# Optimization experiments

Hardware: AMD Instinct MI355X
Metric: run time of the kernel (lower is better)

## Reference

```python
import jax, jax.numpy as jnp
import numpy as np

B, N, T, C = 16, 12, 128, 128  # batch, num_classes (nodes), temporal, channels


def _bn(x, gamma, beta, eps=1e-5):
    # BatchNorm2d in training mode: stats over (batch, t, c), channel axis 1, biased var
    mean = jnp.mean(x, axis=(0, 2, 3), keepdims=True)
    var = jnp.var(x, axis=(0, 2, 3), keepdims=True)
    xn = (x - mean) * jax.lax.rsqrt(var + eps)
    return xn * gamma[None, :, None, None] + beta[None, :, None, None]


def setup_inputs() -> dict:
    key = jax.random.key(0)
    ks = jax.random.split(key, 3)
    scale = np.float32(np.sqrt(2.0 / C))
    inp = {
        'x': jax.random.normal(ks[0], (B, N, T, C), dtype=jnp.float32),
        'edge': jax.random.normal(ks[1], (B, N * N, T, C), dtype=jnp.float32),
    }
    wk = jax.random.split(ks[2], 10)
    for name, k in zip(['A1', 'B1', 'E1', 'U1', 'V1', 'A2', 'B2', 'E2', 'U2', 'V2'], wk):
        inp[name] = jax.random.normal(k, (C, C), dtype=jnp.float32) * scale
    for name, dim in [('g_e1', N * N), ('b_e1', N * N), ('g_v1', N), ('b_v1', N),
                      ('g_e2', N * N), ('b_e2', N * N), ('g_v2', N), ('b_v2', N)]:
        inp[name] = jnp.ones((dim,), jnp.float32) if name[0] == 'g' else jnp.zeros((dim,), jnp.float32)
    return inp


def _forward(x, edge, A1, B1, E1, U1, V1, A2, B2, E2, U2, V2,
             g_e1, b_e1, g_v1, b_v1, g_e2, b_e2, g_v2, b_v2):
    # create_e_matrix: edge index e = i*N + j; 'end' selects node i, 'start' selects node j.
    # Dense incidence einsums become pure gathers; the transpose einsum is a
    # scatter-add over j, i.e. a reshape + sum.
    i_idx = jnp.repeat(jnp.arange(N), N)  # end-node of each edge
    j_idx = jnp.tile(jnp.arange(N), N)    # start-node of each edge
    b, _, t, c = x.shape

    def layer(x, edge, A, Bw, E, U, V, ge, be, gv, bv, mask_node):
        res = x
        edge_upd = (x @ A.T)[:, i_idx] + (x @ Bw.T)[:, j_idx] + edge @ E.T
        edge_upd = _bn(edge_upd, ge, be)
        edge_upd = jnp.where(jnp.isnan(edge_upd), 0.0, edge_upd)
        edge = edge + jax.nn.relu(edge_upd)
        e = jax.nn.sigmoid(edge)
        e = jax.nn.softmax(e.reshape(b, N, N, t, c), axis=2).reshape(b, N * N, t, c)
        Ujx = (x @ V.T)[:, j_idx]
        agg = (e * Ujx).reshape(b, N, N, t, c).sum(axis=2) / N  # scatter to end nodes
        xn = _bn(x @ U.T + agg, gv, bv)
        if mask_node:  # original only NaN-masks node BN in layer 1
            xn = jnp.where(jnp.isnan(xn), 0.0, xn)
        return jax.nn.relu(res + xn), edge

    x, edge = layer(x, edge, A1, B1, E1, U1, V1, g_e1, b_e1, g_v1, b_v1, True)
    x, edge = layer(x, edge, A2, B2, E2, U2, V2, g_e2, b_e2, g_v2, b_v2, False)
    return x, edge


def reference(x, edge, A1, B1, E1, U1, V1, A2, B2, E2, U2, V2,
              g_e1, b_e1, g_v1, b_v1, g_e2, b_e2, g_v2, b_v2):
    return _forward(x, edge, A1, B1, E1, U1, V1, A2, B2, E2, U2, V2,
                    g_e1, b_e1, g_v1, b_v1, g_e2, b_e2, g_v2, b_v2)
```

## Files before the change

kernel.cpp:

```cpp
#include <hip/hip_runtime.h>
#include <hip/hip_bf16.h>

#define BB 16
#define NN 12
#define NE 144
#define TT 128
#define CC 128

typedef __attribute__((ext_vector_type(8))) short v8s;
typedef __attribute__((ext_vector_type(4))) short v4s;
typedef __attribute__((ext_vector_type(4))) float v4f;

__device__ __forceinline__ short f2bf(float f) {
    unsigned u = __float_as_uint(f);
    u += 0x7fffu + ((u >> 16) & 1u);
    return (short)(u >> 16);
}
__device__ __forceinline__ float bf2f(unsigned short u) {
    return __uint_as_float(((unsigned)u) << 16);
}
__device__ __forceinline__ v4s f4_to_bf4(float4 a) {
    v4s r; r[0] = f2bf(a.x); r[1] = f2bf(a.y); r[2] = f2bf(a.z); r[3] = f2bf(a.w); return r;
}

__global__ __launch_bounds__(256) void kW(
    const float* A1, const float* B1, const float* E1, const float* U1, const float* V1,
    const float* A2, const float* B2, const float* E2, const float* U2, const float* V2,
    unsigned short* wb)
{
    int idx = blockIdx.x * 256 + threadIdx.x;
    int w = idx >> 14, r = idx & 16383;
    const float* s;
    switch (w) {
        case 0: s = A1; break; case 1: s = B1; break; case 2: s = E1; break;
        case 3: s = U1; break; case 4: s = V1; break; case 5: s = A2; break;
        case 6: s = B2; break; case 7: s = E2; break; case 8: s = U2; break;
        default: s = V2; break;
    }
    wb[idx] = (unsigned short)f2bf(s[r]);
}

__global__ __launch_bounds__(256) void kP(
    const float* __restrict__ x, const unsigned short* __restrict__ wb,
    int sA, int sB, int sV, int sU,
    unsigned short* __restrict__ oA, unsigned short* __restrict__ oB,
    unsigned short* __restrict__ oV, unsigned short* __restrict__ oU)
{
    __shared__ unsigned short xt[64][136];
    int tid = threadIdx.x;
    int m0 = blockIdx.x * 64;
    #pragma unroll
    for (int it = 0; it < 8; ++it) {
        int f = it * 256 + tid;
        int row = f >> 5, c4 = f & 31;
        float4 v = *reinterpret_cast<const float4*>(x + (size_t)m0 * 128 + (size_t)f * 4);
        *reinterpret_cast<v4s*>(&xt[row][c4 * 4]) = f4_to_bf4(v);
    }
    __syncthreads();
    int lane = tid & 63, wid = tid >> 6;
    int l15 = lane & 15, l4 = lane >> 4;

    const unsigned short* Ws[4] = { wb + (size_t)sA * 16384, wb + (size_t)sB * 16384,
                                    wb + (size_t)sV * 16384, wb + (size_t)sU * 16384 };
    unsigned short* Os[4] = { oA, oB, oV, oU };

    #pragma unroll
    for (int w = 0; w < 4; ++w) {
        const unsigned short* W = Ws[w];
        unsigned short* out = Os[w];
        v8s bfr[2][4];
        #pragma unroll
        for (int nt2 = 0; nt2 < 2; ++nt2) {
            int col = (wid * 2 + nt2) * 16 + l15;
            #pragma unroll
            for (int kk = 0; kk < 4; ++kk)
                bfr[nt2][kk] = *reinterpret_cast<const v8s*>(W + col * 128 + kk * 32 + l4 * 8);
        }
        v4f acc[4][2] = {};
        #pragma unroll
        for (int kk = 0; kk < 4; ++kk) {
            #pragma unroll
            for (int mt = 0; mt < 4; ++mt) {
                v8s a = *reinterpret_cast<const v8s*>(&xt[mt * 16 + l15][kk * 32 + l4 * 8]);
                acc[mt][0] = __builtin_amdgcn_mfma_f32_16x16x32_bf16(a, bfr[0][kk], acc[mt][0], 0, 0, 0);
                acc[mt][1] = __builtin_amdgcn_mfma_f32_16x16x32_bf16(a, bfr[1][kk], acc[mt][1], 0, 0, 0);
            }
        }
        #pragma unroll
        for (int mt = 0; mt < 4; ++mt) {
            #pragma unroll
            for (int nt2 = 0; nt2 < 2; ++nt2) {
                int col = (wid * 2 + nt2) * 16 + l15;
                #pragma unroll
                for (int reg = 0; reg < 4; ++reg) {
                    int rowg = m0 + mt * 16 + l4 * 4 + reg;
                    out[(size_t)rowg * 128 + col] = (unsigned short)f2bf(acc[mt][nt2][reg]);
                }
            }
        }
    }
}

template<bool IN_F32>
__global__ __launch_bounds__(256) void kA(
    const float* __restrict__ ef32, const unsigned short* __restrict__ ebf_in,
    unsigned short* __restrict__ ebf_out,
    unsigned short* __restrict__ updg,
    const unsigned short* __restrict__ xAp, const unsigned short* __restrict__ xBp,
    const unsigned short* __restrict__ Ebf, float2* __restrict__ epart)
{
    __shared__ unsigned short et[64][136];
    __shared__ unsigned short xs[64][136];
    __shared__ float sblk[2];
    int tid = threadIdx.x;
    int bid = blockIdx.x;
    int th = bid & 1;  int m = bid >> 1;
    int e = m % NE, b = m / NE;
    int iA = e / 12, jA = e - iA * 12;
    int t0 = th * 64;
    if (tid < 2) sblk[tid] = 0.f;

    size_t erow0 = ((size_t)(b * NE + e) * TT + t0) * CC;
    if constexpr (IN_F32) {
        #pragma unroll
        for (int it = 0; it < 8; ++it) {
            int f = it * 256 + tid;
            int row = f >> 5, c4 = f & 31;
            float4 v = *reinterpret_cast<const float4*>(ef32 + erow0 + (size_t)row * CC + c4 * 4);
            *reinterpret_cast<v4s*>(&et[row][c4 * 4]) = f4_to_bf4(v);
        }
    } else {
        #pragma unroll
        for (int it = 0; it < 4; ++it) {
            int f = it * 256 + tid;
            int row = f >> 4, c8 = f & 15;
            *reinterpret_cast<v8s*>(&et[row][c8 * 8]) =
                *reinterpret_cast<const v8s*>(ebf_in + erow0 + (size_t)row * CC + c8 * 8);
        }
    }
    {
        size_t xarow = ((size_t)(b * NN + iA) * TT + t0) * CC;
        size_t xbrow = ((size_t)(b * NN + jA) * TT + t0) * CC;
        #pragma unroll
        for (int it = 0; it < 4; ++it) {
            int f = it * 256 + tid;
            int row = f >> 4, c8 = f & 15;
            v8s av = *reinterpret_cast<const v8s*>(xAp + xarow + (size_t)row * CC + c8 * 8);
            v8s bv = *reinterpret_cast<const v8s*>(xBp + xbrow + (size_t)row * CC + c8 * 8);
            v8s sv;
            #pragma unroll
            for (int k = 0; k < 8; ++k)
                sv[k] = f2bf(bf2f((unsigned short)av[k]) + bf2f((unsigned short)bv[k]));
            *reinterpret_cast<v8s*>(&xs[row][c8 * 8]) = sv;
        }
    }
    __syncthreads();
    if constexpr (IN_F32) {
        #pragma unroll
        for (int it = 0; it < 4; ++it) {
            int f = it * 256 + tid;
            int row = f >> 4, c8 = f & 15;
            *reinterpret_cast<v8s*>(ebf_out + erow0 + (size_t)row * CC + c8 * 8) =
                *reinterpret_cast<const v8s*>(&et[row][c8 * 8]);
        }
    }
    int lane = tid & 63, wid = tid >> 6;
    int l15 = lane & 15, l4 = lane >> 4;
    v8s bfr[2][4];
    #pragma unroll
    for (int nt2 = 0; nt2 < 2; ++nt2) {
        int col = (wid * 2 + nt2) * 16 + l15;
        #pragma unroll
        for (int kk = 0; kk < 4; ++kk)
            bfr[nt2][kk] = *reinterpret_cast<const v8s*>(Ebf + col * 128 + kk * 32 + l4 * 8);
    }
    v4f acc[4][2] = {};
    #pragma unroll
    for (int kk = 0; kk < 4; ++kk) {
        #pragma unroll
        for (int mt = 0; mt < 4; ++mt) {
            v8s a = *reinterpret_cast<const v8s*>(&et[mt * 16 + l15][kk * 32 + l4 * 8]);
            acc[mt][0] = __builtin_amdgcn_mfma_f32_16x16x32_bf16(a, bfr[0][kk], acc[mt][0], 0, 0, 0);
            acc[mt][1] = __builtin_amdgcn_mfma_f32_16x16x32_bf16(a, bfr[1][kk], acc[mt][1], 0, 0, 0);
        }
    }
    float s = 0.f, q = 0.f;
    #pragma unroll
    for (int mt = 0; mt < 4; ++mt) {
        #pragma unroll
        for (int nt2 = 0; nt2 < 2; ++nt2) {
            int col = (wid * 2 + nt2) * 16 + l15;
            #pragma unroll
            for (int reg = 0; reg < 4; ++reg) {
                int row = mt * 16 + l4 * 4 + reg;
                float v = acc[mt][nt2][reg] + bf2f(xs[row][col]);
                s += v; q += v * v;
                updg[erow0 + (size_t)row * CC + col] = (unsigned short)f2bf(v);
            }
        }
    }
    #pragma unroll
    for (int off = 1; off < 64; off <<= 1) { s += __shfl_xor(s, off); q += __shfl_xor(q, off); }
    if (lane == 0) { atomicAdd(&sblk[0], s); atomicAdd(&sblk[1], q); }
    __syncthreads();
    if (tid == 0) epart[bid] = make_float2(sblk[0], sblk[1]);
}

__global__ __launch_bounds__(64) void kRede(
    const float2* __restrict__ epart, const float* __restrict__ g,
    const float* __restrict__ be, float* __restrict__ estats)
{
    int e = blockIdx.x;
    int tid = threadIdx.x;
    float s = 0.f, q = 0.f;
    if (tid < 32) {
        int b = tid >> 1, th = tid & 1;
        float2 p = epart[(size_t)((b * NE + e) * 2 + th)];
        s = p.x; q = p.y;
    }
    #pragma unroll
    for (int off = 1; off < 32; off <<= 1) { s += __shfl_xor(s, off); q += __shfl_xor(q, off); }
    if (tid == 0) {
        const float M = 262144.f;
        float mean = s / M;
        float var = q / M - mean * mean;
        float sc = g[e] * rsqrtf(var + 1e-5f);
        estats[e * 2] = sc;
        estats[e * 2 + 1] = be[e] - mean * sc;
    }
}

template<bool OUT_F32>
__global__ __launch_bounds__(256) void kC(
    unsigned short* __restrict__ ebf,
    float* __restrict__ eout,
    const unsigned short* __restrict__ updg,
    const unsigned short* __restrict__ xV, const unsigned short* __restrict__ xU,
    const float* __restrict__ estats,
    unsigned short* __restrict__ yout, float* __restrict__ npart)
{
    __shared__ unsigned short rb[48][136];
    __shared__ unsigned short xv[12][136];
    __shared__ float2 scf[48];
    __shared__ float ns[4], nq[4];
    int tid = threadIdx.x;
    int bid = blockIdx.x;
    int third = bid % 3; int bt = bid / 3;
    int b = bt >> 7, t = bt & 127;
    if (tid < 48) scf[tid] = make_float2(estats[(third * 48 + tid) * 2],
                                         estats[(third * 48 + tid) * 2 + 1]);
    if (tid < 4) { ns[tid] = 0.f; nq[tid] = 0.f; }
    if (tid < 192) {
        int row = tid >> 4, c8 = tid & 15;
        *reinterpret_cast<v8s*>(&xv[row][c8 * 8]) =
            *reinterpret_cast<const v8s*>(xV + (((size_t)(b * NN + row) * TT) + t) * CC + c8 * 8);
    }
    __syncthreads();
    int lane = tid & 63;
    #pragma unroll
    for (int it = 0; it < 3; ++it) {
        int f = it * 256 + tid;
        int row = f >> 4, c8 = f & 15;
        int eg = third * 48 + row;
        size_t goff = (((size_t)(b * NE + eg) * TT) + t) * CC + c8 * 8;
        v8s uv = *reinterpret_cast<const v8s*>(updg + goff);
        v8s ev = *reinterpret_cast<const v8s*>(ebf + goff);
        float2 sc = scf[row];
        float en[8]; v8s nv;
        #pragma unroll
        for (int k = 0; k < 8; ++k) {
            float bn = fmaxf(sc.x * bf2f((unsigned short)uv[k]) + sc.y, 0.f);
            en[k] = bf2f((unsigned short)ev[k]) + bn;
            nv[k] = f2bf(en[k]);
        }
        *reinterpret_cast<v8s*>(&rb[row][c8 * 8]) = nv;
        if constexpr (OUT_F32) {
            *reinterpret_cast<float4*>(eout + goff)     = make_float4(en[0], en[1], en[2], en[3]);
            *reinterpret_cast<float4*>(eout + goff + 4) = make_float4(en[4], en[5], en[6], en[7]);
        } else {
            *reinterpret_cast<v8s*>(ebf + goff) = nv;
        }
    }
    __syncthreads();
    #pragma unroll
    for (int ph = 0; ph < 2; ++ph) {
        int u = tid + ph * 256;
        int il = u >> 7, c = u & 127;
        float den = 0.f, ag = 0.f;
        #pragma unroll
        for (int j = 0; j < 12; ++j) {
            float sv = bf2f(rb[il * 12 + j][c]);
            float sg = 1.f / (1.f + __expf(-sv));
            float ev = __expf(sg);
            den += ev;
            ag += ev * bf2f(xv[j][c]);
        }
        float agg = ag / (den * 12.f);
        int i = third * 4 + il;
        size_t xa = (((size_t)(b * NN + i) * TT) + t) * CC + c;
        float yv = bf2f(xU[xa]) + agg;
        unsigned short us = (unsigned short)f2bf(yv);
        yout[xa] = us;
        float yr = bf2f(us);
        float s1 = yr, s2 = yr * yr;
        #pragma unroll
        for (int off = 1; off < 64; off <<= 1) { s1 += __shfl_xor(s1, off); s2 += __shfl_xor(s2, off); }
        if (lane == 0) { atomicAdd(&ns[il], s1); atomicAdd(&nq[il], s2); }
    }
    __syncthreads();
    if (tid < 4) {
        npart[(size_t)bid * 8 + tid * 2 + 0] = ns[tid];
        npart[(size_t)bid * 8 + tid * 2 + 1] = nq[tid];
    }
}

__global__ __launch_bounds__(256) void kRedn(
    const float* __restrict__ npart, const float* __restrict__ g,
    const float* __restrict__ be, float* __restrict__ nstats)
{
    int n = blockIdx.x;
    int third = n >> 2, il = n & 3;
    float s = 0.f, q = 0.f;
    for (int bt = threadIdx.x; bt < 2048; bt += 256) {
        const float* p = npart + ((size_t)(bt * 3 + third) * 8 + il * 2);
        s += p[0]; q += p[1];
    }
    __shared__ float ss[4], qq[4];
    #pragma unroll
    for (int off = 32; off >= 1; off >>= 1) { s += __shfl_down(s, off); q += __shfl_down(q, off); }
    int wid = threadIdx.x >> 6;
    if ((threadIdx.x & 63) == 0) { ss[wid] = s; qq[wid] = q; }
    __syncthreads();
    if (threadIdx.x == 0) {
        s = ss[0] + ss[1] + ss[2] + ss[3];
        q = qq[0] + qq[1] + qq[2] + qq[3];
        const float M = 262144.f;
        float mean = s / M;
        float var = q / M - mean * mean;
        float sc = g[n] * rsqrtf(var + 1e-5f);
        nstats[n * 2] = sc;
        nstats[n * 2 + 1] = be[n] - mean * sc;
    }
}

__global__ __launch_bounds__(256) void kE(
    const float* xres, const unsigned short* __restrict__ yin,
    const float* __restrict__ nstats, float* xout)
{
    int idx4 = blockIdx.x * 256 + threadIdx.x;
    size_t base = (size_t)idx4 * 4;
    int n = (int)((base >> 14) % 12);
    float scv = nstats[n * 2], shv = nstats[n * 2 + 1];
    float4 xvv = *reinterpret_cast<const float4*>(xres + base);
    v4s yv4 = *reinterpret_cast<const v4s*>(yin + base);
    float4 o;
    o.x = fmaxf(xvv.x + scv * bf2f((unsigned short)yv4[0]) + shv, 0.f);
    o.y = fmaxf(xvv.y + scv * bf2f((unsigned short)yv4[1]) + shv, 0.f);
    o.z = fmaxf(xvv.z + scv * bf2f((unsigned short)yv4[2]) + shv, 0.f);
    o.w = fmaxf(xvv.w + scv * bf2f((unsigned short)yv4[3]) + shv, 0.f);
    *reinterpret_cast<float4*>(xout + base) = o;
}

extern "C" void kernel_launch(void* const* d_in, const int* in_sizes, int n_in,
                              void* d_out, int out_size, void* d_ws, size_t ws_size,
                              hipStream_t stream)
{
    const float* x0 = (const float*)d_in[0];
    const float* e0 = (const float*)d_in[1];
    const float* W[10];
    for (int i = 0; i < 10; ++i) W[i] = (const float*)d_in[2 + i];
    const float* ge1 = (const float*)d_in[12];
    const float* be1 = (const float*)d_in[13];
    const float* gv1 = (const float*)d_in[14];
    const float* bv1 = (const float*)d_in[15];
    const float* ge2 = (const float*)d_in[16];
    const float* be2 = (const float*)d_in[17];
    const float* gv2 = (const float*)d_in[18];
    const float* bv2 = (const float*)d_in[19];

    const size_t SZX = (size_t)BB * NN * TT * CC;
    const size_t SZE = (size_t)BB * NE * TT * CC;
    float* out_x = (float*)d_out;
    float* out_e = out_x + SZX;

    unsigned short* ws16 = (unsigned short*)d_ws;
    unsigned short* xA = ws16;
    unsigned short* xB = ws16 + SZX;
    unsigned short* xV = ws16 + 2 * SZX;
    unsigned short* xU = ws16 + 3 * SZX;
    unsigned short* yb = ws16 + 4 * SZX;
    unsigned short* ebf = ws16 + 5 * SZX;
    unsigned short* upd = ebf + SZE;
    float2* epart  = (float2*)(upd + SZE);
    float* estats = (float*)(epart + 4608);
    float* npart  = estats + 288;
    float* nstats = npart + 49152;
    unsigned short* wb = (unsigned short*)(nstats + 24);

    float* x1 = out_x;

    kW<<<640, 256, 0, stream>>>(W[0], W[1], W[2], W[3], W[4], W[5], W[6], W[7], W[8], W[9], wb);

    kP<<<384, 256, 0, stream>>>(x0, wb, 0, 1, 4, 3, xA, xB, xV, xU);
    kA<true><<<4608, 256, 0, stream>>>(e0, nullptr, ebf, upd, xA, xB, wb + 2 * 16384, epart);
    kRede<<<144, 64, 0, stream>>>(epart, ge1, be1, estats);
    kC<false><<<6144, 256, 0, stream>>>(ebf, nullptr, upd, xV, xU, estats, yb, npart);
    kRedn<<<12, 256, 0, stream>>>(npart, gv1, bv1, nstats);
    kE<<<3072, 256, 0, stream>>>(x0, yb, nstats, x1);

    kP<<<384, 256, 0, stream>>>(x1, wb, 5, 6, 9, 8, xA, xB, xV, xU);
    kA<false><<<4608, 256, 0, stream>>>(nullptr, ebf, nullptr, upd, xA, xB, wb + 7 * 16384, epart);
    kRede<<<144, 64, 0, stream>>>(epart, ge2, be2, estats);
    kC<true><<<6144, 256, 0, stream>>>(ebf, out_e, upd, xV, xU, estats, yb, npart);
    kRedn<<<12, 256, 0, stream>>>(npart, gv2, bv2, nstats);
    kE<<<3072, 256, 0, stream>>>(x1, yb, nstats, out_x);
}
```

Measured before the change: 297.3 us.

## Transpose edge GEMM in kA, halve tile rows, drop xs staging buffer

The edge-update kernel now processes 32 time rows per block instead of 64, which doubles the grid to 9216 blocks. It swaps the MFMA operand roles so the edge tile in LDS is the B operand and the weight matrix E is read directly from global as the A operand. Each lane then holds 4 contiguous output channels, so updg writes and the xA/xB loads become 8-byte vector accesses. The shared xs buffer and its precomputed sum are removed, and xA+xB are read straight from global in the epilogue, which cuts LDS use and raises occupancy. The trade-offs are repeated global reads of E per block, more partial stats, and a slightly different rounding (xA+xB is no longer rounded to bf16 before the add).

```diff
diff --git a/kernel.cpp b/kernel.cpp
--- a/kernel.cpp
+++ b/kernel.cpp
@@ -109,21 +109,20 @@
     const unsigned short* __restrict__ xAp, const unsigned short* __restrict__ xBp,
     const unsigned short* __restrict__ Ebf, float2* __restrict__ epart)
 {
-    __shared__ unsigned short et[64][136];
-    __shared__ unsigned short xs[64][136];
+    __shared__ unsigned short et[32][136];
     __shared__ float sblk[2];
     int tid = threadIdx.x;
     int bid = blockIdx.x;
-    int th = bid & 1;  int m = bid >> 1;
+    int th = bid & 3; int m = bid >> 2;
     int e = m % NE, b = m / NE;
     int iA = e / 12, jA = e - iA * 12;
-    int t0 = th * 64;
+    int t0 = th * 32;
     if (tid < 2) sblk[tid] = 0.f;
-
     size_t erow0 = ((size_t)(b * NE + e) * TT + t0) * CC;
+
     if constexpr (IN_F32) {
         #pragma unroll
-        for (int it = 0; it < 8; ++it) {
+        for (int it = 0; it < 4; ++it) {
             int f = it * 256 + tid;
             int row = f >> 5, c4 = f & 31;
             float4 v = *reinterpret_cast<const float4*>(ef32 + erow0 + (size_t)row * CC + c4 * 4);
@@ -131,33 +130,17 @@
         }
     } else {
         #pragma unroll
-        for (int it = 0; it < 4; ++it) {
+        for (int it = 0; it < 2; ++it) {
             int f = it * 256 + tid;
             int row = f >> 4, c8 = f & 15;
             *reinterpret_cast<v8s*>(&et[row][c8 * 8]) =
                 *reinterpret_cast<const v8s*>(ebf_in + erow0 + (size_t)row * CC + c8 * 8);
         }
     }
-    {
-        size_t xarow = ((size_t)(b * NN + iA) * TT + t0) * CC;
-        size_t xbrow = ((size_t)(b * NN + jA) * TT + t0) * CC;
-        #pragma unroll
-        for (int it = 0; it < 4; ++it) {
-            int f = it * 256 + tid;
-            int row = f >> 4, c8 = f & 15;
-            v8s av = *reinterpret_cast<const v8s*>(xAp + xarow + (size_t)row * CC + c8 * 8);
-            v8s bv = *reinterpret_cast<const v8s*>(xBp + xbrow + (size_t)row * CC + c8 * 8);
-            v8s sv;
-            #pragma unroll
-            for (int k = 0; k < 8; ++k)
-                sv[k] = f2bf(bf2f((unsigned short)av[k]) + bf2f((unsigned short)bv[k]));
-            *reinterpret_cast<v8s*>(&xs[row][c8 * 8]) = sv;
-        }
-    }
     __syncthreads();
     if constexpr (IN_F32) {
         #pragma unroll
-        for (int it = 0; it < 4; ++it) {
+        for (int it = 0; it < 2; ++it) {
             int f = it * 256 + tid;
             int row = f >> 4, c8 = f & 15;
             *reinterpret_cast<v8s*>(ebf_out + erow0 + (size_t)row * CC + c8 * 8) =
@@ -166,38 +149,41 @@
     }
     int lane = tid & 63, wid = tid >> 6;
     int l15 = lane & 15, l4 = lane >> 4;
-    v8s bfr[2][4];
-    #pragma unroll
-    for (int nt2 = 0; nt2 < 2; ++nt2) {
-        int col = (wid * 2 + nt2) * 16 + l15;
-        #pragma unroll
-        for (int kk = 0; kk < 4; ++kk)
-            bfr[nt2][kk] = *reinterpret_cast<const v8s*>(Ebf + col * 128 + kk * 32 + l4 * 8);
-    }
-    v4f acc[4][2] = {};
-    #pragma unroll
-    for (int kk = 0; kk < 4; ++kk) {
-        #pragma unroll
-        for (int mt = 0; mt < 4; ++mt) {
-            v8s a = *reinterpret_cast<const v8s*>(&et[mt * 16 + l15][kk * 32 + l4 * 8]);
-            acc[mt][0] = __builtin_amdgcn_mfma_f32_16x16x32_bf16(a, bfr[0][kk], acc[mt][0], 0, 0, 0);
-            acc[mt][1] = __builtin_amdgcn_mfma_f32_16x16x32_bf16(a, bfr[1][kk], acc[mt][1], 0, 0, 0);
-        }
-    }
+    int nt = wid & 1;
+    int mb = (wid >> 1) * 4;
+    int tl = nt * 16 + l15;
+
+    v8s bf[4];
+    #pragma unroll
+    for (int kk = 0; kk < 4; ++kk)
+        bf[kk] = *reinterpret_cast<const v8s*>(&et[tl][kk * 32 + l4 * 8]);
+
+    v4f acc[4] = {};
+    #pragma unroll
+    for (int mm = 0; mm < 4; ++mm) {
+        #pragma unroll
+        for (int kk = 0; kk < 4; ++kk) {
+            v8s a = *reinterpret_cast<const v8s*>(
+                Ebf + (size_t)((mb + mm) * 16 + l15) * 128 + kk * 32 + l4 * 8);
+            acc[mm] = __builtin_amdgcn_mfma_f32_16x16x32_bf16(a, bf[kk], acc[mm], 0, 0, 0);
+        }
+    }
+    size_t xarow = ((size_t)(b * NN + iA) * TT + t0 + tl) * CC;
+    size_t xbrow = ((size_t)(b * NN + jA) * TT + t0 + tl) * CC;
     float s = 0.f, q = 0.f;
     #pragma unroll
-    for (int mt = 0; mt < 4; ++mt) {
-        #pragma unroll
-        for (int nt2 = 0; nt2 < 2; ++nt2) {
-            int col = (wid * 2 + nt2) * 16 + l15;
-            #pragma unroll
-            for (int reg = 0; reg < 4; ++reg) {
-                int row = mt * 16 + l4 * 4 + reg;
-                float v = acc[mt][nt2][reg] + bf2f(xs[row][col]);
-                s += v; q += v * v;
-                updg[erow0 + (size_t)row * CC + col] = (unsigned short)f2bf(v);
-            }
-        }
+    for (int mm = 0; mm < 4; ++mm) {
+        int c0 = (mb + mm) * 16 + l4 * 4;
+        v4s xa = *reinterpret_cast<const v4s*>(xAp + xarow + c0);
+        v4s xb = *reinterpret_cast<const v4s*>(xBp + xbrow + c0);
+        v4s outv;
+        #pragma unroll
+        for (int reg = 0; reg < 4; ++reg) {
+            float v = acc[mm][reg] + bf2f((unsigned short)xa[reg]) + bf2f((unsigned short)xb[reg]);
+            s += v; q += v * v;
+            outv[reg] = f2bf(v);
+        }
+        *reinterpret_cast<v4s*>(updg + erow0 + (size_t)tl * CC + c0) = outv;
     }
     #pragma unroll
     for (int off = 1; off < 64; off <<= 1) { s += __shfl_xor(s, off); q += __shfl_xor(q, off); }
@@ -212,14 +198,11 @@
 {
     int e = blockIdx.x;
     int tid = threadIdx.x;
-    float s = 0.f, q = 0.f;
-    if (tid < 32) {
-        int b = tid >> 1, th = tid & 1;
-        float2 p = epart[(size_t)((b * NE + e) * 2 + th)];
-        s = p.x; q = p.y;
-    }
-    #pragma unroll
-    for (int off = 1; off < 32; off <<= 1) { s += __shfl_xor(s, off); q += __shfl_xor(q, off); }
+    int b = tid >> 2, th = tid & 3;
+    float2 p = epart[(size_t)(b * NE + e) * 4 + th];
+    float s = p.x, q = p.y;
+    #pragma unroll
+    for (int off = 1; off < 64; off <<= 1) { s += __shfl_xor(s, off); q += __shfl_xor(q, off); }
     if (tid == 0) {
         const float M = 262144.f;
         float mean = s / M;
@@ -392,7 +375,7 @@
     unsigned short* ebf = ws16 + 5 * SZX;
     unsigned short* upd = ebf + SZE;
     float2* epart  = (float2*)(upd + SZE);
-    float* estats = (float*)(epart + 4608);
+    float* estats = (float*)(epart + 9216);
     float* npart  = estats + 288;
     float* nstats = npart + 49152;
     unsigned short* wb = (unsigned short*)(nstats + 24);
@@ -402,14 +385,14 @@
     kW<<<640, 256, 0, stream>>>(W[0], W[1], W[2], W[3], W[4], W[5], W[6], W[7], W[8], W[9], wb);
 
     kP<<<384, 256, 0, stream>>>(x0, wb, 0, 1, 4, 3, xA, xB, xV, xU);
-    kA<true><<<4608, 256, 0, stream>>>(e0, nullptr, ebf, upd, xA, xB, wb + 2 * 16384, epart);
+    kA<true><<<9216, 256, 0, stream>>>(e0, nullptr, ebf, upd, xA, xB, wb + 2 * 16384, epart);
     kRede<<<144, 64, 0, stream>>>(epart, ge1, be1, estats);
     kC<false><<<6144, 256, 0, stream>>>(ebf, nullptr, upd, xV, xU, estats, yb, npart);
     kRedn<<<12, 256, 0, stream>>>(npart, gv1, bv1, nstats);
     kE<<<3072, 256, 0, stream>>>(x0, yb, nstats, x1);
 
     kP<<<384, 256, 0, stream>>>(x1, wb, 5, 6, 9, 8, xA, xB, xV, xU);
-    kA<false><<<4608, 256, 0, stream>>>(nullptr, ebf, nullptr, upd, xA, xB, wb + 7 * 16384, epart);
+    kA<false><<<9216, 256, 0, stream>>>(nullptr, ebf, nullptr, upd, xA, xB, wb + 7 * 16384, epart);
     kRede<<<144, 64, 0, stream>>>(epart, ge2, be2, estats);
     kC<true><<<6144, 256, 0, stream>>>(ebf, out_e, upd, xV, xU, estats, yb, npart);
     kRedn<<<12, 256, 0, stream>>>(npart, gv2, bv2, nstats);
```

Result: slower. 428.1 us (+44.0%).

## Restage edge-update kernel to coalesce output stores and drop xs LDS buffer

Applied to the files above, without the earlier changes.

The edge-update kernel no longer stages the summed node projections in a second LDS tile. Instead the MFMA result is written back into the edge tile in LDS and reread row-major, so the xA/xB gather-add, the BN statistics and the bf16 output store all become 16-byte vectorized, coalesced accesses instead of scattered 2-byte stores. The bf16 edge copy is written directly during the fp32 load, and launch bounds request 4 blocks per CU. The cost is an extra LDS round trip and two more barriers. The result is now rounded to bf16 before the add, which slightly changes numerics.

```diff
diff --git a/kernel.cpp b/kernel.cpp
--- a/kernel.cpp
+++ b/kernel.cpp
@@ -102,7 +102,7 @@
 }
 
 template<bool IN_F32>
-__global__ __launch_bounds__(256) void kA(
+__global__ __launch_bounds__(256, 4) void kA(
     const float* __restrict__ ef32, const unsigned short* __restrict__ ebf_in,
     unsigned short* __restrict__ ebf_out,
     unsigned short* __restrict__ updg,
@@ -110,24 +110,25 @@
     const unsigned short* __restrict__ Ebf, float2* __restrict__ epart)
 {
     __shared__ unsigned short et[64][136];
-    __shared__ unsigned short xs[64][136];
     __shared__ float sblk[2];
     int tid = threadIdx.x;
     int bid = blockIdx.x;
-    int th = bid & 1;  int m = bid >> 1;
+    int th = bid & 1; int m = bid >> 1;
     int e = m % NE, b = m / NE;
     int iA = e / 12, jA = e - iA * 12;
     int t0 = th * 64;
     if (tid < 2) sblk[tid] = 0.f;
-
     size_t erow0 = ((size_t)(b * NE + e) * TT + t0) * CC;
+
     if constexpr (IN_F32) {
         #pragma unroll
         for (int it = 0; it < 8; ++it) {
             int f = it * 256 + tid;
             int row = f >> 5, c4 = f & 31;
             float4 v = *reinterpret_cast<const float4*>(ef32 + erow0 + (size_t)row * CC + c4 * 4);
-            *reinterpret_cast<v4s*>(&et[row][c4 * 4]) = f4_to_bf4(v);
+            v4s bv = f4_to_bf4(v);
+            *reinterpret_cast<v4s*>(&et[row][c4 * 4]) = bv;
+            *reinterpret_cast<v4s*>(ebf_out + erow0 + (size_t)row * CC + c4 * 4) = bv;
         }
     } else {
         #pragma unroll
@@ -138,34 +139,11 @@
                 *reinterpret_cast<const v8s*>(ebf_in + erow0 + (size_t)row * CC + c8 * 8);
         }
     }
-    {
-        size_t xarow = ((size_t)(b * NN + iA) * TT + t0) * CC;
-        size_t xbrow = ((size_t)(b * NN + jA) * TT + t0) * CC;
-        #pragma unroll
-        for (int it = 0; it < 4; ++it) {
-            int f = it * 256 + tid;
-            int row = f >> 4, c8 = f & 15;
-            v8s av = *reinterpret_cast<const v8s*>(xAp + xarow + (size_t)row * CC + c8 * 8);
-            v8s bv = *reinterpret_cast<const v8s*>(xBp + xbrow + (size_t)row * CC + c8 * 8);
-            v8s sv;
-            #pragma unroll
-            for (int k = 0; k < 8; ++k)
-                sv[k] = f2bf(bf2f((unsigned short)av[k]) + bf2f((unsigned short)bv[k]));
-            *reinterpret_cast<v8s*>(&xs[row][c8 * 8]) = sv;
-        }
-    }
-    __syncthreads();
-    if constexpr (IN_F32) {
-        #pragma unroll
-        for (int it = 0; it < 4; ++it) {
-            int f = it * 256 + tid;
-            int row = f >> 4, c8 = f & 15;
-            *reinterpret_cast<v8s*>(ebf_out + erow0 + (size_t)row * CC + c8 * 8) =
-                *reinterpret_cast<const v8s*>(&et[row][c8 * 8]);
-        }
-    }
+    __syncthreads();
+
     int lane = tid & 63, wid = tid >> 6;
     int l15 = lane & 15, l4 = lane >> 4;
+
     v8s bfr[2][4];
     #pragma unroll
     for (int nt2 = 0; nt2 < 2; ++nt2) {
@@ -184,20 +162,37 @@
             acc[mt][1] = __builtin_amdgcn_mfma_f32_16x16x32_bf16(a, bfr[1][kk], acc[mt][1], 0, 0, 0);
         }
     }
-    float s = 0.f, q = 0.f;
+    __syncthreads();
     #pragma unroll
     for (int mt = 0; mt < 4; ++mt) {
         #pragma unroll
         for (int nt2 = 0; nt2 < 2; ++nt2) {
             int col = (wid * 2 + nt2) * 16 + l15;
             #pragma unroll
-            for (int reg = 0; reg < 4; ++reg) {
-                int row = mt * 16 + l4 * 4 + reg;
-                float v = acc[mt][nt2][reg] + bf2f(xs[row][col]);
-                s += v; q += v * v;
-                updg[erow0 + (size_t)row * CC + col] = (unsigned short)f2bf(v);
-            }
-        }
+            for (int reg = 0; reg < 4; ++reg)
+                et[mt * 16 + l4 * 4 + reg][col] = (unsigned short)f2bf(acc[mt][nt2][reg]);
+        }
+    }
+    __syncthreads();
+    size_t xaoff = ((size_t)(b * NN + iA) * TT + t0) * CC;
+    size_t xboff = ((size_t)(b * NN + jA) * TT + t0) * CC;
+    float s = 0.f, q = 0.f;
+    #pragma unroll
+    for (int it = 0; it < 4; ++it) {
+        int f = it * 256 + tid;
+        int row = f >> 4, c8 = f & 15;
+        v8s ev = *reinterpret_cast<const v8s*>(&et[row][c8 * 8]);
+        v8s xa = *reinterpret_cast<const v8s*>(xAp + xaoff + (size_t)row * CC + c8 * 8);
+        v8s xb = *reinterpret_cast<const v8s*>(xBp + xboff + (size_t)row * CC + c8 * 8);
+        v8s outv;
+        #pragma unroll
+        for (int k = 0; k < 8; ++k) {
+            float v = bf2f((unsigned short)ev[k]) + bf2f((unsigned short)xa[k])
+                    + bf2f((unsigned short)xb[k]);
+            s += v; q += v * v;
+            outv[k] = f2bf(v);
+        }
+        *reinterpret_cast<v8s*>(updg + erow0 + (size_t)row * CC + c8 * 8) = outv;
     }
     #pragma unroll
     for (int off = 1; off < 64; off <<= 1) { s += __shfl_xor(s, off); q += __shfl_xor(q, off); }
@@ -215,7 +210,7 @@
     float s = 0.f, q = 0.f;
     if (tid < 32) {
         int b = tid >> 1, th = tid & 1;
-        float2 p = epart[(size_t)((b * NE + e) * 2 + th)];
+        float2 p = epart[(size_t)(b * NE + e) * 2 + th];
         s = p.x; q = p.y;
     }
     #pragma unroll
```

Result: faster. 285.2 us (-4.1%).
